# Optimization experiments

Measured on AMD Instinct MI355X. Metric: run time of the kernel, lower is better.

The kernel has to match this reference:

```python
import jax, jax.numpy as jnp
import numpy as np

N_NODES = 100000
N_EDGES = 600000
IN_FEAT = 128
OUT_FEAT = 128
REL_NUM = 5


def setup_inputs() -> dict:
    key = jax.random.key(0)
    k = jax.random.split(key, 7)
    h = jax.random.normal(k[0], (N_NODES, IN_FEAT), dtype=jnp.float32)
    weight = jax.random.normal(k[1], (REL_NUM, IN_FEAT, OUT_FEAT), dtype=jnp.float32)
    W_0 = jax.random.normal(k[2], (IN_FEAT, OUT_FEAT), dtype=jnp.float32)
    norm = jax.random.uniform(k[3], (N_EDGES,), dtype=jnp.float32)
    src = jax.random.randint(k[4], (N_EDGES,), 0, N_NODES, dtype=jnp.int32)
    dst = jax.random.randint(k[5], (N_EDGES,), 0, N_NODES, dtype=jnp.int32)
    edge_id = jax.random.randint(k[6], (N_EDGES,), 0, REL_NUM, dtype=jnp.int32)
    return {"h": h, "weight": weight, "W_0": W_0, "norm": norm,
            "src": src, "dst": dst, "edge_id": edge_id}


def reference(h, weight, W_0, norm, src, dst, edge_id):
    # Per-edge msg = h[src] @ weight[edge_id] * norm.
    # Equivalent, efficient form: transform all nodes by every relation weight
    # once (R is small), then gather per edge instead of materializing an
    # [E, in, out] weight tensor.
    all_h = jnp.einsum('ni,rio->rno', h, weight)          # [R, N, out]
    msg = all_h[edge_id, src] * norm[:, None]             # [E, out]
    h_sum = jax.ops.segment_sum(msg, dst, num_segments=h.shape[0])  # [N, out]
    out = jax.nn.relu(h @ W_0 + h_sum)                    # [N, out]
    return out
```

## Files before the change

### kernel.cpp

```cpp
#include <hip/hip_runtime.h>
#include <hip/hip_bf16.h>


#define NN   100000
#define NE   600000
#define FEAT 128
#define RNUM 5
#define CAP  32
#define KC   24

#define SCAT_B 2344
#define PREP_T (NN * 32 + FEAT * KC * 32)
#define PREP_B ((PREP_T + 255) / 256)

typedef __attribute__((ext_vector_type(8))) short short8;
typedef __attribute__((ext_vector_type(4))) float float4v;

static __device__ __forceinline__ unsigned short f2bf(float x) {
  union { float f; unsigned u; } v; v.f = x;
  unsigned r = v.u + 0x7FFFu + ((v.u >> 16) & 1u);
  return (unsigned short)(r >> 16);
}

__global__ void k_prep(const int* __restrict__ src, const int* __restrict__ dst,
                       const int* __restrict__ eid, const float* __restrict__ norm,
                       const float* __restrict__ h, const float* __restrict__ weight,
                       const float* __restrict__ W0, int* __restrict__ cnt,
                       int2* __restrict__ s_edge, unsigned short* __restrict__ hb,
                       unsigned short* __restrict__ Bt) {
  int bid = blockIdx.x;
  if (bid < SCAT_B) {
    int e = bid * 256 + threadIdx.x;
    if (e < NE) {
      int d = dst[e];
      int p = atomicAdd(&cnt[d], 1);
      if (p < CAP) {
        union { float f; int i; } nb; nb.f = norm[e];
        s_edge[(size_t)d * CAP + p] = make_int2(src[e] | (eid[e] << 20), nb.i);
      }
    }
  } else {
    int t = (bid - SCAT_B) * 256 + threadIdx.x;
    if (t < NN * 32) {
      float4v v = *(const float4v*)(h + (size_t)t * 4);
      unsigned long long p = (unsigned long long)f2bf(v[0])
                           | ((unsigned long long)f2bf(v[1]) << 16)
                           | ((unsigned long long)f2bf(v[2]) << 32)
                           | ((unsigned long long)f2bf(v[3]) << 48);
      *(unsigned long long*)(hb + (size_t)t * 4) = p;
    } else {
      int u = t - NN * 32;
      if (u < FEAT * KC * 32) {
        int j = u & 7, g = u >> 3;
        int ln = g & 63, n0 = (g >> 6) & 7, c = g >> 9;
        int o = n0 * 16 + (ln & 15);
        int k = c * 32 + ((ln >> 4) << 3) + j;
        float v = (k < 640) ? weight[(k >> 7) * 16384 + (k & 127) * 128 + o]
                            : W0[(k - 640) * 128 + o];
        Bt[u] = f2bf(v);
      }
    }
  }
}

static __device__ __forceinline__ void accum_edge(float acc[RNUM][8], int2 e,
                                                  uint4 v) {
  union { int i; float f; } nb; nb.i = e.y;
  int r = e.x >> 20;
  float nm[RNUM];
#pragma unroll
  for (int rr = 0; rr < RNUM; ++rr) nm[rr] = (r == rr) ? nb.f : 0.f;
  float f[8];
  unsigned w[4] = {v.x, v.y, v.z, v.w};
#pragma unroll
  for (int d = 0; d < 4; ++d) {
    union { unsigned u; float g; } lo, hi;
    lo.u = w[d] << 16; hi.u = w[d] & 0xFFFF0000u;
    f[2 * d] = lo.g; f[2 * d + 1] = hi.g;
  }
#pragma unroll
  for (int rr = 0; rr < RNUM; ++rr)
#pragma unroll
    for (int i = 0; i < 8; ++i) acc[rr][i] += nm[rr] * f[i];
}

__global__ __launch_bounds__(512, 6) void k_fused(
    const unsigned short* __restrict__ hb, const int* __restrict__ cnt,
    const int2* __restrict__ s_edge, const unsigned short* __restrict__ Bt,
    float* __restrict__ out) {
  __shared__ uint4 Atile[2 * KC * 64];
  int tid = threadIdx.x;
  int wv = tid >> 6, lane = tid & 63;
  int g = lane >> 4, t = lane & 15;
  int base = blockIdx.x * 32;
  int node = base + wv * 4 + g;
  int row = (wv & 3) * 4 + g;
  uint4* Aw = Atile + (wv >> 2) * (KC * 64);
  const uint4* hb4 = (const uint4*)hb;

  int glen = cnt[node]; if (glen > CAP) glen = CAP;
  const int2* ep = s_edge + (size_t)node * CAP;
  float acc[RNUM][8] = {};
  int j = 0;
  for (; j + 2 <= glen; j += 2) {
    int2 e0 = ep[j], e1 = ep[j + 1];
    uint4 v0 = hb4[(e0.x & 0xFFFFF) * 16 + t];
    uint4 v1 = hb4[(e1.x & 0xFFFFF) * 16 + t];
    accum_edge(acc, e0, v0);
    accum_edge(acc, e1, v1);
  }
  if (j < glen) {
    int2 e = ep[j];
    uint4 v = hb4[(e.x & 0xFFFFF) * 16 + t];
    accum_edge(acc, e, v);
  }
  int q = t & 3, cb = t >> 2;
#pragma unroll
  for (int rr = 0; rr < RNUM; ++rr) {
    int c = rr * 4 + cb;
    uint4 pk;
    pk.x = (unsigned)f2bf(acc[rr][0]) | ((unsigned)f2bf(acc[rr][1]) << 16);
    pk.y = (unsigned)f2bf(acc[rr][2]) | ((unsigned)f2bf(acc[rr][3]) << 16);
    pk.z = (unsigned)f2bf(acc[rr][4]) | ((unsigned)f2bf(acc[rr][5]) << 16);
    pk.w = (unsigned)f2bf(acc[rr][6]) | ((unsigned)f2bf(acc[rr][7]) << 16);
    Aw[c * 64 + q * 16 + (row ^ ((c * 4 + q) & 7))] = pk;
  }
  {
    int c = 20 + cb;
    Aw[c * 64 + q * 16 + (row ^ ((c * 4 + q) & 7))] = hb4[(size_t)node * 16 + t];
  }
  __syncthreads();

  int m = lane & 15, qq = lane >> 4;
  float4v cacc[2];
  cacc[0] = (float4v){0.f, 0.f, 0.f, 0.f};
  cacc[1] = (float4v){0.f, 0.f, 0.f, 0.f};
#pragma unroll
  for (int c = 0; c < KC; ++c) {
    int sx = qq * 16 + (m ^ ((c * 4 + qq) & 7));
    short8 af0 = *(const short8*)&Atile[c * 64 + sx];
    short8 af1 = *(const short8*)&Atile[KC * 64 + c * 64 + sx];
    short8 bf  = *(const short8*)&Bt[((c * 8 + wv) * 64 + lane) * 8];
    cacc[0] = __builtin_amdgcn_mfma_f32_16x16x32_bf16(af0, bf, cacc[0], 0, 0, 0);
    cacc[1] = __builtin_amdgcn_mfma_f32_16x16x32_bf16(af1, bf, cacc[1], 0, 0, 0);
  }
#pragma unroll
  for (int tt = 0; tt < 2; ++tt) {
#pragma unroll
    for (int r = 0; r < 4; ++r) {
      int rrow = base + tt * 16 + qq * 4 + r;
      float v = cacc[tt][r];
      out[(size_t)rrow * FEAT + wv * 16 + m] = v > 0.f ? v : 0.f;
    }
  }
}

__global__ void k_slow_mm(const float* __restrict__ h, const float* __restrict__ W0,
                          float* __restrict__ out) {
  __shared__ float hn[128];
  int n = blockIdx.x, t = threadIdx.x;
  hn[t] = h[(size_t)n * 128 + t];
  __syncthreads();
  float a = 0.f;
  for (int i = 0; i < 128; ++i) a += hn[i] * W0[i * 128 + t];
  out[(size_t)n * 128 + t] = a;
}
__global__ void k_slow_edge(const float* __restrict__ h, const float* __restrict__ weight,
                            const float* __restrict__ norm, const int* __restrict__ src,
                            const int* __restrict__ dst, const int* __restrict__ eid,
                            float* __restrict__ out) {
  __shared__ float hs[128];
  int e = blockIdx.x, t = threadIdx.x;
  hs[t] = h[(size_t)src[e] * 128 + t];
  __syncthreads();
  const float* W = weight + (size_t)eid[e] * 16384;
  float a = 0.f;
  for (int i = 0; i < 128; ++i) a += hs[i] * W[i * 128 + t];
  atomicAdd(&out[(size_t)dst[e] * 128 + t], a * norm[e]);
}
__global__ void k_slow_relu(float* out) {
  int i = blockIdx.x * 256 + threadIdx.x;
  if (i < NN * FEAT) out[i] = fmaxf(out[i], 0.f);
}

extern "C" void kernel_launch(void* const* d_in, const int* in_sizes, int n_in,
                              void* d_out, int out_size, void* d_ws, size_t ws_size,
                              hipStream_t stream) {
  const float* h      = (const float*)d_in[0];
  const float* weight = (const float*)d_in[1];
  const float* W0     = (const float*)d_in[2];
  const float* norm   = (const float*)d_in[3];
  const int*   src    = (const int*)d_in[4];
  const int*   dst    = (const int*)d_in[5];
  const int*   eid    = (const int*)d_in[6];
  float* out = (float*)d_out;

  char* ws = (char*)d_ws;
  size_t off = 0;
  auto wsalloc = [&](size_t bytes) -> char* {
    char* p = ws + off;
    off += (bytes + 255) & ~(size_t)255;
    return p;
  };
  unsigned short* hb  = (unsigned short*)wsalloc((size_t)NN * FEAT * 2);
  unsigned short* Bt  = (unsigned short*)wsalloc((size_t)FEAT * KC * 32 * 2);
  int*   cnt      = (int*)wsalloc((size_t)NN * 4);
  int2*  s_edge   = (int2*)wsalloc((size_t)NN * CAP * 8 + 256);

  if (ws_size >= off) {
    hipMemsetAsync(cnt, 0, (size_t)NN * 4, stream);
    k_prep <<<SCAT_B + PREP_B, 256, 0, stream>>>(src, dst, eid, norm, h, weight,
                                                 W0, cnt, s_edge, hb, Bt);
    k_fused<<<NN / 32, 512, 0, stream>>>(hb, cnt, s_edge, Bt, out);
  } else {
    k_slow_mm  <<<NN, 128, 0, stream>>>(h, W0, out);
    k_slow_edge<<<NE, 128, 0, stream>>>(h, weight, norm, src, dst, eid, out);
    k_slow_relu<<<(NN * FEAT + 255) / 256, 256, 0, stream>>>(out);
  }
}
```

Measured before the change: 204.5 us.

## Stage output through LDS for coalesced stores and read self features from global

The ReLU output is staged through shared memory so each thread writes two contiguous float4 vectors instead of scattered scalar stores. The self-feature (h @ W0) K-chunks are now loaded from global memory straight into MFMA fragments rather than copied into the LDS tile, which shrinks the tile from 24 to 20 chunks per half. Edge pairs are read with one int4 load. The cost is two extra block barriers and a padded LDS staging area reused from the A tile.

```diff
diff --git a/kernel.cpp b/kernel.cpp
--- a/kernel.cpp
+++ b/kernel.cpp
@@ -8,6 +8,7 @@
 #define RNUM 5
 #define CAP  32
 #define KC   24
+#define KCL  20
 
 #define SCAT_B 2344
 #define PREP_T (NN * 32 + FEAT * KC * 32)
@@ -88,14 +89,14 @@
     const unsigned short* __restrict__ hb, const int* __restrict__ cnt,
     const int2* __restrict__ s_edge, const unsigned short* __restrict__ Bt,
     float* __restrict__ out) {
-  __shared__ uint4 Atile[2 * KC * 64];
+  __shared__ uint4 Atile[2 * KCL * 64];
   int tid = threadIdx.x;
   int wv = tid >> 6, lane = tid & 63;
   int g = lane >> 4, t = lane & 15;
   int base = blockIdx.x * 32;
   int node = base + wv * 4 + g;
   int row = (wv & 3) * 4 + g;
-  uint4* Aw = Atile + (wv >> 2) * (KC * 64);
+  uint4* Aw = Atile + (wv >> 2) * (KCL * 64);
   const uint4* hb4 = (const uint4*)hb;
 
   int glen = cnt[node]; if (glen > CAP) glen = CAP;
@@ -103,7 +104,8 @@
   float acc[RNUM][8] = {};
   int j = 0;
   for (; j + 2 <= glen; j += 2) {
-    int2 e0 = ep[j], e1 = ep[j + 1];
+    int4 ee = *(const int4*)(ep + j);
+    int2 e0 = make_int2(ee.x, ee.y), e1 = make_int2(ee.z, ee.w);
     uint4 v0 = hb4[(e0.x & 0xFFFFF) * 16 + t];
     uint4 v1 = hb4[(e1.x & 0xFFFFF) * 16 + t];
     accum_edge(acc, e0, v0);
@@ -125,10 +127,6 @@
     pk.w = (unsigned)f2bf(acc[rr][6]) | ((unsigned)f2bf(acc[rr][7]) << 16);
     Aw[c * 64 + q * 16 + (row ^ ((c * 4 + q) & 7))] = pk;
   }
-  {
-    int c = 20 + cb;
-    Aw[c * 64 + q * 16 + (row ^ ((c * 4 + q) & 7))] = hb4[(size_t)node * 16 + t];
-  }
   __syncthreads();
 
   int m = lane & 15, qq = lane >> 4;
@@ -136,23 +134,39 @@
   cacc[0] = (float4v){0.f, 0.f, 0.f, 0.f};
   cacc[1] = (float4v){0.f, 0.f, 0.f, 0.f};
 #pragma unroll
-  for (int c = 0; c < KC; ++c) {
+  for (int c = 0; c < KCL; ++c) {
     int sx = qq * 16 + (m ^ ((c * 4 + qq) & 7));
     short8 af0 = *(const short8*)&Atile[c * 64 + sx];
-    short8 af1 = *(const short8*)&Atile[KC * 64 + c * 64 + sx];
+    short8 af1 = *(const short8*)&Atile[KCL * 64 + c * 64 + sx];
     short8 bf  = *(const short8*)&Bt[((c * 8 + wv) * 64 + lane) * 8];
     cacc[0] = __builtin_amdgcn_mfma_f32_16x16x32_bf16(af0, bf, cacc[0], 0, 0, 0);
     cacc[1] = __builtin_amdgcn_mfma_f32_16x16x32_bf16(af1, bf, cacc[1], 0, 0, 0);
   }
 #pragma unroll
-  for (int tt = 0; tt < 2; ++tt) {
+  for (int c = KCL; c < KC; ++c) {
+    short8 bf = *(const short8*)&Bt[((c * 8 + wv) * 64 + lane) * 8];
+    short8 a0 = *(const short8*)&hb4[(size_t)(base + m) * 16 + (c - KCL) * 4 + qq];
+    short8 a1 = *(const short8*)&hb4[(size_t)(base + 16 + m) * 16 + (c - KCL) * 4 + qq];
+    cacc[0] = __builtin_amdgcn_mfma_f32_16x16x32_bf16(a0, bf, cacc[0], 0, 0, 0);
+    cacc[1] = __builtin_amdgcn_mfma_f32_16x16x32_bf16(a1, bf, cacc[1], 0, 0, 0);
+  }
+
+  __syncthreads();
+  float* Cs = (float*)Atile;
+#pragma unroll
+  for (int tt = 0; tt < 2; ++tt)
 #pragma unroll
     for (int r = 0; r < 4; ++r) {
-      int rrow = base + tt * 16 + qq * 4 + r;
       float v = cacc[tt][r];
-      out[(size_t)rrow * FEAT + wv * 16 + m] = v > 0.f ? v : 0.f;
+      Cs[(tt * 16 + qq * 4 + r) * 132 + wv * 16 + m] = v > 0.f ? v : 0.f;
     }
-  }
+  __syncthreads();
+  int r0 = tid >> 4, c0 = (tid & 15) * 8;
+  float4v w0 = *(const float4v*)&Cs[r0 * 132 + c0];
+  float4v w1 = *(const float4v*)&Cs[r0 * 132 + c0 + 4];
+  float* op = out + (size_t)(base + r0) * FEAT + c0;
+  *(float4v*)op = w0;
+  *(float4v*)(op + 4) = w1;
 }
 
 __global__ void k_slow_mm(const float* __restrict__ h, const float* __restrict__ W0,
```

New measurement: 217.5 us. 1.06x slower.

## Load edge lists via lane shuffles, unroll gather, stage output through LDS

Applied to the files above, without the earlier changes.

Each 16-lane group loads its node's whole edge list with one vector load and broadcasts entries via shuffles, then gathers four neighbor rows at once to raise memory-level parallelism. The epilogue writes ReLU results into shared memory and stores full rows with coalesced float4 writes. Occupancy hint is lowered to allow more registers for the unrolled gather. Adds extra barriers and loop iterations up to the group's max degree.

```diff
diff --git a/kernel.cpp b/kernel.cpp
--- a/kernel.cpp
+++ b/kernel.cpp
@@ -63,10 +63,10 @@
   }
 }
 
-static __device__ __forceinline__ void accum_edge(float acc[RNUM][8], int2 e,
-                                                  uint4 v) {
-  union { int i; float f; } nb; nb.i = e.y;
-  int r = e.x >> 20;
+static __device__ __forceinline__ void accum_edge(float acc[RNUM][8], int ex,
+                                                  int ey, uint4 v) {
+  union { int i; float f; } nb; nb.i = ey;
+  int r = ex >> 20;
   float nm[RNUM];
 #pragma unroll
   for (int rr = 0; rr < RNUM; ++rr) nm[rr] = (r == rr) ? nb.f : 0.f;
@@ -84,7 +84,7 @@
     for (int i = 0; i < 8; ++i) acc[rr][i] += nm[rr] * f[i];
 }
 
-__global__ __launch_bounds__(512, 6) void k_fused(
+__global__ __launch_bounds__(512, 5) void k_fused(
     const unsigned short* __restrict__ hb, const int* __restrict__ cnt,
     const int2* __restrict__ s_edge, const unsigned short* __restrict__ Bt,
     float* __restrict__ out) {
@@ -100,20 +100,31 @@
 
   int glen = cnt[node]; if (glen > CAP) glen = CAP;
   const int2* ep = s_edge + (size_t)node * CAP;
+  uint4 ee = ((const uint4*)ep)[t];
+  int wmax = glen;
+  wmax = max(wmax, __shfl_xor(wmax, 16));
+  wmax = max(wmax, __shfl_xor(wmax, 32));
+  int sl0 = lane & 48;
+
   float acc[RNUM][8] = {};
-  int j = 0;
-  for (; j + 2 <= glen; j += 2) {
-    int2 e0 = ep[j], e1 = ep[j + 1];
-    uint4 v0 = hb4[(e0.x & 0xFFFFF) * 16 + t];
-    uint4 v1 = hb4[(e1.x & 0xFFFFF) * 16 + t];
-    accum_edge(acc, e0, v0);
-    accum_edge(acc, e1, v1);
-  }
-  if (j < glen) {
-    int2 e = ep[j];
-    uint4 v = hb4[(e.x & 0xFFFFF) * 16 + t];
-    accum_edge(acc, e, v);
-  }
+  for (int j = 0; j < wmax; j += 4) {
+    int ex[4], ey[4];
+#pragma unroll
+    for (int u = 0; u < 4; ++u) {
+      int jj = j + u;
+      int sl = sl0 + (jj >> 1);
+      ex[u] = __shfl((jj & 1) ? (int)ee.z : (int)ee.x, sl);
+      ey[u] = __shfl((jj & 1) ? (int)ee.w : (int)ee.y, sl);
+    }
+    uint4 v[4];
+#pragma unroll
+    for (int u = 0; u < 4; ++u)
+      if (j + u < glen) v[u] = hb4[(ex[u] & 0xFFFFF) * 16 + t];
+#pragma unroll
+    for (int u = 0; u < 4; ++u)
+      if (j + u < glen) accum_edge(acc, ex[u], ey[u], v[u]);
+  }
+
   int q = t & 3, cb = t >> 2;
 #pragma unroll
   for (int rr = 0; rr < RNUM; ++rr) {
@@ -144,15 +155,23 @@
     cacc[0] = __builtin_amdgcn_mfma_f32_16x16x32_bf16(af0, bf, cacc[0], 0, 0, 0);
     cacc[1] = __builtin_amdgcn_mfma_f32_16x16x32_bf16(af1, bf, cacc[1], 0, 0, 0);
   }
-#pragma unroll
-  for (int tt = 0; tt < 2; ++tt) {
+
+  __syncthreads();
+  float* Cs = (float*)Atile;
+#pragma unroll
+  for (int tt = 0; tt < 2; ++tt)
 #pragma unroll
     for (int r = 0; r < 4; ++r) {
-      int rrow = base + tt * 16 + qq * 4 + r;
       float v = cacc[tt][r];
-      out[(size_t)rrow * FEAT + wv * 16 + m] = v > 0.f ? v : 0.f;
-    }
-  }
+      Cs[(tt * 16 + qq * 4 + r) * 132 + wv * 16 + m] = v > 0.f ? v : 0.f;
+    }
+  __syncthreads();
+  int r0 = tid >> 4, c0 = (tid & 15) * 8;
+  float4v w0 = *(const float4v*)&Cs[r0 * 132 + c0];
+  float4v w1 = *(const float4v*)&Cs[r0 * 132 + c0 + 4];
+  float* op = out + (size_t)(base + r0) * FEAT + c0;
+  *(float4v*)op = w0;
+  *(float4v*)(op + 4) = w1;
 }
 
 __global__ void k_slow_mm(const float* __restrict__ h, const float* __restrict__ W0,
```

New measurement: 328.5 us. 1.61x slower.
